# Kernel optimization log

Hardware: AMD Instinct MI355X
Metric: run time of the kernel (lower is better)

The kernel has to match this reference:

```python
import jax, jax.numpy as jnp
import numpy as np

N, E, D, H, O, L = 50000, 400000, 128, 128, 64, 2


def setup_inputs() -> dict:
    key = jax.random.key(0)
    ks = jax.random.split(key, 24)
    s = 0.05
    rn = lambda k, shape: jax.random.normal(k, shape, jnp.float32) * s
    # random edges with no self-loops (dst = src + nonzero offset mod N)
    src = jax.random.randint(ks[0], (E,), 0, N, dtype=jnp.int32)
    off = jax.random.randint(ks[1], (E,), 1, N, dtype=jnp.int32)
    dst = (src + off) % N
    edge_index = jnp.stack([src, dst])  # [2, E] int32
    return {
        "x": rn(ks[2], (N, D)),
        "edge_index": edge_index,
        "attn_W": rn(ks[3], (L, 2 * D, 2)),
        "attn_b": rn(ks[4], (L, 2)),
        "mlp_W1": rn(ks[5], (L, D, H)),
        "mlp_b1": rn(ks[6], (L, H)),
        "mlp_W2": rn(ks[7], (L, H, H)),
        "mlp_b2": rn(ks[8], (L, H)),
        "bn_gamma": jnp.ones((L, H), jnp.float32),   # torch BatchNorm1d default affine init
        "bn_beta": jnp.zeros((L, H), jnp.float32),
        "gru_Wih": rn(ks[9], (D, 3 * H)),
        "gru_Whh": rn(ks[10], (H, 3 * H)),
        "gru_bih": rn(ks[11], (3 * H,)),
        "gru_bhh": rn(ks[12], (3 * H,)),
        "last_W1": rn(ks[13], (H, H)),
        "last_b1": rn(ks[14], (H,)),
        "last_W2": rn(ks[15], (H, O)),
        "last_b2": rn(ks[16], (O,)),
    }


def reference(x, edge_index, attn_W, attn_b, mlp_W1, mlp_b1, mlp_W2, mlp_b2,
              bn_gamma, bn_beta, gru_Wih, gru_Whh, gru_bih, gru_bhh,
              last_W1, last_b1, last_W2, last_b2):
    n = x.shape[0]
    # symmetrize edge list: message (nbr -> node) for both directions
    node = jnp.concatenate([edge_index[0], edge_index[1]])  # destination
    nbr = jnp.concatenate([edge_index[1], edge_index[0]])   # source / neighbor
    deg = jax.ops.segment_sum(jnp.ones((node.shape[0], 1), x.dtype), node, num_segments=n)
    has_nbr = deg > 0

    h_state = jnp.zeros((n, gru_Whh.shape[0]), x.dtype)
    for l in range(attn_W.shape[0]):
        feats = x[nbr]  # [2E, d] gather
        s_agg = jax.ops.segment_sum(feats, node, num_segments=n)
        m_agg = jax.ops.segment_max(feats, node, num_segments=n)
        m_agg = jnp.where(has_nbr, m_agg, jnp.zeros_like(m_agg))  # isolated nodes stay 0
        # attention over {sum, max} aggregations
        scores = jnp.concatenate([s_agg, m_agg], axis=1) @ attn_W[l] + attn_b[l]  # [n, 2]
        w = jax.nn.softmax(scores, axis=1)
        comb = x + w[:, :1] * s_agg + w[:, 1:] * m_agg
        # MLP (in -> hidden, ReLU, hidden -> out)
        z = jax.nn.relu(comb @ mlp_W1[l] + mlp_b1[l]) @ mlp_W2[l] + mlp_b2[l]
        # BatchNorm1d in eval mode with running stats (mean 0, var 1): affine only
        z = z * bn_gamma[l] + bn_beta[l]
        # GRUCell
        gi = z @ gru_Wih + gru_bih
        gh = h_state @ gru_Whh + gru_bhh
        ir, iz, inn = jnp.split(gi, 3, axis=1)
        hr, hz, hn = jnp.split(gh, 3, axis=1)
        r = jax.nn.sigmoid(ir + hr)
        u = jax.nn.sigmoid(iz + hz)
        ncand = jnp.tanh(inn + r * hn)
        h_state = (1.0 - u) * ncand + u * h_state
        x = h_state
    # final node-level MLP
    out = jax.nn.relu(x @ last_W1 + last_b1) @ last_W2 + last_b2
    return out
```

## Files before the change

kernel.cpp:

```cpp
#include <hip/hip_runtime.h>
#include <math.h>

typedef unsigned short u16;
typedef __attribute__((ext_vector_type(8))) short bf16x8;
typedef __attribute__((ext_vector_type(4))) float f32x4;

#define ADJ_CAP 96

__device__ __forceinline__ u16 f2b(float f) {
    union { float f; unsigned u; } v; v.f = f;
    unsigned r = (v.u + 0x7FFF + ((v.u >> 16) & 1)) >> 16;
    return (u16)r;
}
__device__ __forceinline__ float b2f(u16 h) {
    union { unsigned u; float f; } v; v.u = (unsigned)h << 16;
    return v.f;
}
__device__ __forceinline__ float u2f(unsigned u) {
    union { unsigned u; float f; } v; v.u = u;
    return v.f;
}
__device__ __forceinline__ float fsig(float x) { return 1.f / (1.f + __expf(-x)); }
__device__ __forceinline__ float ftanh(float x) {
    float e = __expf(2.f * x);
    return 1.f - 2.f / (e + 1.f);
}

__device__ __forceinline__ void gll16(const void* g, void* l) {
    __builtin_amdgcn_global_load_lds(
        (const __attribute__((address_space(1))) void*)g,
        (__attribute__((address_space(3))) void*)l, 16, 0, 0);
}

__device__ __forceinline__ void conv_chunk(const float* __restrict__ src,
                                           u16* __restrict__ dst, int c, int NC) {
    int sl = c / NC, n = c - sl * NC;
    u16 tmp[8];
#pragma unroll
    for (int i = 0; i < 8; ++i) tmp[i] = f2b(src[(size_t)(sl * 8 + i) * NC + n]);
    *(uint4*)(dst + (size_t)c * 8) = *(const uint4*)tmp;
}

__global__ void k_pro(const int* __restrict__ ei, int* __restrict__ cnt,
                      u16* __restrict__ adj, int E, int N,
                      const float* __restrict__ W1, const float* __restrict__ W2,
                      const float* __restrict__ Wih, const float* __restrict__ Whh,
                      const float* __restrict__ lW1, const float* __restrict__ lW2,
                      u16* __restrict__ tW1, u16* __restrict__ tW2,
                      u16* __restrict__ tGRU,
                      u16* __restrict__ tlW1, u16* __restrict__ tlW2, int L,
                      const float* __restrict__ x, u16* __restrict__ xb, int n8) {
    const int EB = (E + 255) >> 8;
    const int nwc = L * 4096 + 12288 + 3072;
    const int WB = (nwc + 255) >> 8;
    int b = blockIdx.x;
    if (b < EB * 8) {
        const int part = b & 7, chunk = b >> 3;
        const int span = (N + 7) >> 3;
        const int nlo = part * span;
        const int nhi = (nlo + span < N) ? nlo + span : N;
        int e = chunk * 256 + threadIdx.x;
        if (e < E) {
            int s = __builtin_nontemporal_load(&ei[e]);
            int d = __builtin_nontemporal_load(&ei[E + e]);
            if (s >= nlo && s < nhi) {
                int p = atomicAdd(&cnt[s], 1);
                adj[(size_t)s * ADJ_CAP + p] = (u16)d;
            }
            if (d >= nlo && d < nhi) {
                int q = atomicAdd(&cnt[d], 1);
                adj[(size_t)d * ADJ_CAP + q] = (u16)s;
            }
        }
        return;
    }
    b -= EB * 8;
    if (b < WB) {
        int c = b * 256 + threadIdx.x;
        if (c >= nwc) return;
        if (c < L * 2048) { int l = c >> 11; conv_chunk(W1 + (size_t)l * 16384, tW1 + (size_t)l * 16384, c & 2047, 128); return; }
        c -= L * 2048;
        if (c < L * 2048) { int l = c >> 11; conv_chunk(W2 + (size_t)l * 16384, tW2 + (size_t)l * 16384, c & 2047, 128); return; }
        c -= L * 2048;
        if (c < 12288) {
            int s = c >> 9, r = c & 511;
            int q = r >> 7, mat = (r >> 6) & 1, cc = r & 63;
            int h = s / 12, s2 = s % 12, kc = s2 / 3, g = s2 % 3;
            int ocol = g * 128 + h * 64 + cc;
            const float* src = mat ? Whh : Wih;
            int kb = (kc * 4 + q) * 8;
            u16 tmp[8];
#pragma unroll
            for (int e = 0; e < 8; ++e) tmp[e] = f2b(src[(size_t)(kb + e) * 384 + ocol]);
            *(uint4*)(tGRU + (size_t)c * 8) = *(const uint4*)tmp;
            return;
        }
        c -= 12288;
        if (c < 2048) { conv_chunk(lW1, tlW1, c, 128); return; }
        c -= 2048;
        if (c < 1024) { conv_chunk(lW2, tlW2, c, 64); return; }
        return;
    }
    b -= WB;
    {
        int i = b * 256 + threadIdx.x;
        if (i < n8) {
            float4 a = *(const float4*)(x + (size_t)i * 8);
            float4 bb = *(const float4*)(x + (size_t)i * 8 + 4);
            u16 t[8] = {f2b(a.x), f2b(a.y), f2b(a.z), f2b(a.w),
                        f2b(bb.x), f2b(bb.y), f2b(bb.z), f2b(bb.w)};
            *(uint4*)(xb + (size_t)i * 8) = *(const uint4*)t;
        }
    }
}

__global__ __launch_bounds__(256) void k_agg(const u16* __restrict__ xb,
                                             const u16* __restrict__ adj,
                                             const int* __restrict__ cnt,
                                             const float* __restrict__ aW,
                                             const float* __restrict__ ab,
                                             u16* __restrict__ comb, int N) {
    int n = blockIdx.x * 4 + (threadIdx.x >> 6);
    if (n >= N) return;
    int l = threadIdx.x & 63;
    int grp = l >> 4;
    int f0 = (l & 15) * 8;
    int beg = n * ADJ_CAP, deg = cnt[n], end = beg + deg;
    float s[8], m[8];
#pragma unroll
    for (int i = 0; i < 8; ++i) { s[i] = 0.f; m[i] = -3.402823e38f; }

    auto acc8 = [&](uint4 v) {
        unsigned d[4] = {v.x, v.y, v.z, v.w};
#pragma unroll
        for (int i = 0; i < 4; ++i) {
            float a0 = u2f(d[i] << 16);
            float a1 = u2f(d[i] & 0xFFFF0000u);
            s[2 * i] += a0;     m[2 * i] = fmaxf(m[2 * i], a0);
            s[2 * i + 1] += a1; m[2 * i + 1] = fmaxf(m[2 * i + 1], a1);
        }
    };

    int j = beg + grp;
    for (; j + 4 < end; j += 8) {
        int a0 = adj[j], a1 = adj[j + 4];
        uint4 v0 = *(const uint4*)(xb + (size_t)a0 * 128 + f0);
        uint4 v1 = *(const uint4*)(xb + (size_t)a1 * 128 + f0);
        acc8(v0);
        acc8(v1);
    }
    if (j < end) {
        int a = adj[j];
        uint4 v = *(const uint4*)(xb + (size_t)a * 128 + f0);
        acc8(v);
    }
#pragma unroll
    for (int i = 0; i < 8; ++i) {
        s[i] += __shfl_xor(s[i], 16);
        s[i] += __shfl_xor(s[i], 32);
        m[i] = fmaxf(m[i], __shfl_xor(m[i], 16));
        m[i] = fmaxf(m[i], __shfl_xor(m[i], 32));
    }
    if (deg == 0) {
#pragma unroll
        for (int i = 0; i < 8; ++i) m[i] = 0.f;
    }
    float p0 = 0.f, p1 = 0.f;
#pragma unroll
    for (int i = 0; i < 8; ++i) {
        float2 wS = *(const float2*)(aW + (size_t)(f0 + i) * 2);
        float2 wM = *(const float2*)(aW + (size_t)(128 + f0 + i) * 2);
        p0 += s[i] * wS.x + m[i] * wM.x;
        p1 += s[i] * wS.y + m[i] * wM.y;
    }
#pragma unroll
    for (int o = 8; o; o >>= 1) { p0 += __shfl_xor(p0, o); p1 += __shfl_xor(p1, o); }
    p0 += ab[0]; p1 += ab[1];
    float pm = fmaxf(p0, p1);
    float ea = __expf(p0 - pm), eb = __expf(p1 - pm);
    float w0 = ea / (ea + eb), w1 = 1.f - w0;
    if (grp == 0) {
        uint4 xv = *(const uint4*)(xb + (size_t)n * 128 + f0);
        unsigned xs[4] = {xv.x, xv.y, xv.z, xv.w};
        unsigned dw[4];
#pragma unroll
        for (int i = 0; i < 4; ++i) {
            float xlo = u2f(xs[i] << 16), xhi = u2f(xs[i] & 0xFFFF0000u);
            float olo = xlo + w0 * s[2 * i] + w1 * m[2 * i];
            float ohi = xhi + w0 * s[2 * i + 1] + w1 * m[2 * i + 1];
            dw[i] = (unsigned)f2b(olo) | ((unsigned)f2b(ohi) << 16);
        }
        uint4 o4 = make_uint4(dw[0], dw[1], dw[2], dw[3]);
        *(uint4*)(comb + (size_t)n * 128 + f0) = o4;
    }
}

template <bool H0>
__global__ __launch_bounds__(512, 4) void k_layer(
    const u16* __restrict__ Cb, const u16* __restrict__ Hb,
    const u16* __restrict__ W1t, const float* __restrict__ b1,
    const u16* __restrict__ W2t, const float* __restrict__ b2,
    const float* __restrict__ gam, const float* __restrict__ bet,
    const u16* __restrict__ tG,
    const float* __restrict__ bih, const float* __restrict__ bhh,
    u16* __restrict__ HnB, int M) {
    __shared__ __align__(16) u16 x_s[128 * 16 * 8];
    __shared__ __align__(16) u16 b_s[3][4096];
    const int t = threadIdx.x;
    const int m0 = blockIdx.x * 128;
    const int wid = t >> 6, lane = t & 63, lo = lane & 15, hi = lane >> 4;
    const int arow = 16 * wid + lo;

    auto issue = [&](int s) {
        const u16* g = (s < 4) ? (W1t + (size_t)s * 4096)
                     : (s < 8) ? (W2t + (size_t)(s - 4) * 4096)
                               : (tG + (size_t)(s - 8) * 4096);
        char* l = (char*)b_s[s % 3] + wid * 1024;
        const char* gp = (const char*)g + wid * 1024 + lane * 16;
        gll16(gp, l);
    };

    float b1r[8], g2r[8], t2r[8];
#pragma unroll
    for (int j = 0; j < 8; ++j) {
        int c = 16 * j + lo;
        b1r[j] = b1[c];
        float gv = gam[c];
        g2r[j] = gv;
        t2r[j] = b2[c] * gv + bet[c];
    }
#pragma unroll
    for (int i = 0; i < 4; ++i) {
        int off = (i * 8 + wid) * 1024;
        int row = (off >> 8) + (lane >> 4);
        int sl = lane & 15;
        int gr = m0 + row; gr = gr < M ? gr : M - 1;
        gll16(Cb + (size_t)gr * 128 + ((sl ^ (row & 7)) * 8), (char*)x_s + off);
    }
    issue(0);
    issue(1);

    f32x4 acc[8];
#pragma unroll
    for (int j = 0; j < 8; ++j) acc[j] = (f32x4)0.f;

#pragma unroll
    for (int ks = 0; ks < 4; ++ks) {
        const int p = ks;
        asm volatile("s_waitcnt vmcnt(1)" ::: "memory");
        __builtin_amdgcn_s_barrier();
        issue(p + 2);
        bf16x8 af = *(const bf16x8*)&x_s[(arow * 16 + ((ks * 4 + hi) ^ (arow & 7))) * 8];
        const u16* buf = b_s[p % 3];
        __builtin_amdgcn_s_setprio(1);
#pragma unroll
        for (int j = 0; j < 8; ++j) {
            bf16x8 bf = *(const bf16x8*)&buf[((size_t)hi * 128 + 16 * j + lo) * 8];
            acc[j] = __builtin_amdgcn_mfma_f32_16x16x32_bf16(af, bf, acc[j], 0, 0, 0);
        }
        __builtin_amdgcn_s_setprio(0);
    }
#pragma unroll
    for (int j = 0; j < 8; ++j) {
        int c = 16 * j + lo;
#pragma unroll
        for (int q = 0; q < 4; ++q) {
            int row = 16 * wid + hi * 4 + q;
            float v = fmaxf(acc[j][q] + b1r[j], 0.f);
            int sl = c >> 3;
            x_s[(row * 16 + (sl ^ (row & 7))) * 8 + (c & 7)] = f2b(v);
        }
        acc[j] = (f32x4)0.f;
    }

#pragma unroll
    for (int ks = 0; ks < 4; ++ks) {
        const int p = 4 + ks;
        asm volatile("s_waitcnt vmcnt(1)" ::: "memory");
        __builtin_amdgcn_s_barrier();
        issue(p + 2);
        bf16x8 af = *(const bf16x8*)&x_s[(arow * 16 + ((ks * 4 + hi) ^ (arow & 7))) * 8];
        const u16* buf = b_s[p % 3];
        __builtin_amdgcn_s_setprio(1);
#pragma unroll
        for (int j = 0; j < 8; ++j) {
            bf16x8 bf = *(const bf16x8*)&buf[((size_t)hi * 128 + 16 * j + lo) * 8];
            acc[j] = __builtin_amdgcn_mfma_f32_16x16x32_bf16(af, bf, acc[j], 0, 0, 0);
        }
        __builtin_amdgcn_s_setprio(0);
    }
#pragma unroll
    for (int j = 0; j < 8; ++j) {
        int c = 16 * j + lo;
#pragma unroll
        for (int q = 0; q < 4; ++q) {
            int row = 16 * wid + hi * 4 + q;
            float v = acc[j][q] * g2r[j] + t2r[j];
            int sl = c >> 3;
            x_s[(row * 16 + (sl ^ (row & 7))) * 8 + (c & 7)] = f2b(v);
        }
    }
    bf16x8 hreg[4];
    if (!H0) {
        int gr = m0 + arow; gr = gr < M ? gr : M - 1;
#pragma unroll
        for (int kc = 0; kc < 4; ++kc)
            hreg[kc] = *(const bf16x8*)(Hb + (size_t)gr * 128 + (kc * 4 + hi) * 8);
    }

    f32x4 racc[4], uacc[4], nza[4], nha[4];

    auto epi = [&](int h) {
#pragma unroll
        for (int ct = 0; ct < 4; ++ct) {
            int c = h * 64 + ct * 16 + lo;
            float b_r = bih[c] + bhh[c];
            float b_u = bih[c + 128] + bhh[c + 128];
            float b_in = bih[c + 256], b_hn = bhh[c + 256];
#pragma unroll
            for (int q = 0; q < 4; ++q) {
                int r = m0 + 16 * wid + hi * 4 + q;
                if (r < M) {
                    float rr = fsig(racc[ct][q] + b_r);
                    float uu = fsig(uacc[ct][q] + b_u);
                    float hterm = H0 ? b_hn : (nha[ct][q] + b_hn);
                    float nn = ftanh(nza[ct][q] + b_in + rr * hterm);
                    float hv = H0 ? 0.f : b2f(Hb[(size_t)r * 128 + c]);
                    float o = (1.f - uu) * nn + uu * hv;
                    HnB[(size_t)r * 128 + c] = f2b(o);
                }
            }
        }
    };

#pragma unroll
    for (int h = 0; h < 2; ++h) {
#pragma unroll
        for (int j = 0; j < 4; ++j) {
            racc[j] = (f32x4)0.f; uacc[j] = (f32x4)0.f;
            nza[j] = (f32x4)0.f; nha[j] = (f32x4)0.f;
        }
#pragma unroll
        for (int kc = 0; kc < 4; ++kc) {
            bf16x8 zf;
#pragma unroll
            for (int g = 0; g < 3; ++g) {
                const int p = 8 + h * 12 + kc * 3 + g;
                if (p == 31) asm volatile("s_waitcnt vmcnt(0)" ::: "memory");
                else         asm volatile("s_waitcnt vmcnt(1)" ::: "memory");
                __builtin_amdgcn_s_barrier();
                if (p + 2 <= 31) issue(p + 2);
                if (g == 0)
                    zf = *(const bf16x8*)&x_s[(arow * 16 + ((kc * 4 + hi) ^ (arow & 7))) * 8];
                const u16* buf = b_s[p % 3];
                __builtin_amdgcn_s_setprio(1);
#pragma unroll
                for (int jj = 0; jj < 4; ++jj) {
                    bf16x8 wi = *(const bf16x8*)&buf[((size_t)hi * 128 + jj * 16 + lo) * 8];
                    if (g == 0)      racc[jj] = __builtin_amdgcn_mfma_f32_16x16x32_bf16(zf, wi, racc[jj], 0, 0, 0);
                    else if (g == 1) uacc[jj] = __builtin_amdgcn_mfma_f32_16x16x32_bf16(zf, wi, uacc[jj], 0, 0, 0);
                    else             nza[jj]  = __builtin_amdgcn_mfma_f32_16x16x32_bf16(zf, wi, nza[jj], 0, 0, 0);
                    if (!H0) {
                        bf16x8 wh = *(const bf16x8*)&buf[((size_t)hi * 128 + 64 + jj * 16 + lo) * 8];
                        if (g == 0)      racc[jj] = __builtin_amdgcn_mfma_f32_16x16x32_bf16(hreg[kc], wh, racc[jj], 0, 0, 0);
                        else if (g == 1) uacc[jj] = __builtin_amdgcn_mfma_f32_16x16x32_bf16(hreg[kc], wh, uacc[jj], 0, 0, 0);
                        else             nha[jj]  = __builtin_amdgcn_mfma_f32_16x16x32_bf16(hreg[kc], wh, nha[jj], 0, 0, 0);
                    }
                }
                __builtin_amdgcn_s_setprio(0);
            }
        }
        epi(h);
    }
}

__global__ __launch_bounds__(256, 2) void k_final(const u16* __restrict__ Hb,
                                                  const u16* __restrict__ W1t,
                                                  const float* __restrict__ b1,
                                                  const u16* __restrict__ W2t,
                                                  const float* __restrict__ b2,
                                                  float* __restrict__ out, int M) {
    __shared__ __align__(16) u16 x_s[64 * 16 * 8];
    __shared__ __align__(16) u16 w_s[16 * 128 * 8];
    const int t = threadIdx.x;
    const int m0 = blockIdx.x * 64;
    const int w = t >> 6, l = t & 63, lo = l & 15, hi = l >> 4;
    const int arow = 16 * w + lo;
#pragma unroll
    for (int i = 0; i < 4; ++i) {
        int idx = t + i * 256;
        int row = idx >> 4, sl = idx & 15;
        int gr = m0 + row; gr = gr < M ? gr : M - 1;
        *(uint4*)&x_s[(row * 16 + (sl ^ (row & 7))) * 8] =
            *(const uint4*)(Hb + (size_t)gr * 128 + sl * 8);
    }
#pragma unroll
    for (int i = 0; i < 8; ++i) {
        int idx = t + i * 256;
        *(uint4*)&w_s[idx * 8] = *(const uint4*)(W1t + (size_t)idx * 8);
    }
    __syncthreads();
    f32x4 acc[8];
#pragma unroll
    for (int j = 0; j < 8; ++j) acc[j] = (f32x4)0.f;
#pragma unroll
    for (int ks = 0; ks < 4; ++ks) {
        bf16x8 af = *(const bf16x8*)&x_s[(arow * 16 + ((ks * 4 + hi) ^ (arow & 7))) * 8];
#pragma unroll
        for (int j = 0; j < 8; ++j) {
            bf16x8 bf = *(const bf16x8*)&w_s[((ks * 4 + hi) * 128 + 16 * j + lo) * 8];
            acc[j] = __builtin_amdgcn_mfma_f32_16x16x32_bf16(af, bf, acc[j], 0, 0, 0);
        }
    }
    __syncthreads();
#pragma unroll
    for (int j = 0; j < 8; ++j) {
        int c = 16 * j + lo;
        float bv = b1[c];
#pragma unroll
        for (int q = 0; q < 4; ++q) {
            int row = 16 * w + hi * 4 + q;
            float v = fmaxf(acc[j][q] + bv, 0.f);
            int sl = c >> 3;
            x_s[(row * 16 + (sl ^ (row & 7))) * 8 + (c & 7)] = f2b(v);
        }
    }
#pragma unroll
    for (int i = 0; i < 4; ++i) {
        int idx = t + i * 256;
        *(uint4*)&w_s[idx * 8] = *(const uint4*)(W2t + (size_t)idx * 8);
    }
    __syncthreads();
    f32x4 a2[4];
#pragma unroll
    for (int j = 0; j < 4; ++j) a2[j] = (f32x4)0.f;
#pragma unroll
    for (int ks = 0; ks < 4; ++ks) {
        bf16x8 af = *(const bf16x8*)&x_s[(arow * 16 + ((ks * 4 + hi) ^ (arow & 7))) * 8];
#pragma unroll
        for (int j = 0; j < 4; ++j) {
            bf16x8 bf = *(const bf16x8*)&w_s[((ks * 4 + hi) * 64 + 16 * j + lo) * 8];
            a2[j] = __builtin_amdgcn_mfma_f32_16x16x32_bf16(af, bf, a2[j], 0, 0, 0);
        }
    }
#pragma unroll
    for (int j = 0; j < 4; ++j) {
        int c = 16 * j + lo;
        float bv = b2[c];
#pragma unroll
        for (int q = 0; q < 4; ++q) {
            int r = m0 + 16 * w + hi * 4 + q;
            if (r < M) out[(size_t)r * 64 + c] = a2[j][q] + bv;
        }
    }
}

extern "C" void kernel_launch(void* const* d_in, const int* in_sizes, int n_in,
                              void* d_out, int out_size, void* d_ws, size_t ws_size,
                              hipStream_t stream) {
    const float* x   = (const float*)d_in[0];
    const int*   ei  = (const int*)d_in[1];
    const float* aW  = (const float*)d_in[2];
    const float* ab  = (const float*)d_in[3];
    const float* W1  = (const float*)d_in[4];
    const float* b1  = (const float*)d_in[5];
    const float* W2  = (const float*)d_in[6];
    const float* b2  = (const float*)d_in[7];
    const float* gam = (const float*)d_in[8];
    const float* bet = (const float*)d_in[9];
    const float* Wih = (const float*)d_in[10];
    const float* Whh = (const float*)d_in[11];
    const float* bih = (const float*)d_in[12];
    const float* bhh = (const float*)d_in[13];
    const float* lW1 = (const float*)d_in[14];
    const float* lb1 = (const float*)d_in[15];
    const float* lW2 = (const float*)d_in[16];
    const float* lb2 = (const float*)d_in[17];

    const int N = in_sizes[0] / 128;
    const int E = in_sizes[1] / 2;
    const int L = in_sizes[3] / 2;
    float* out = (float*)d_out;

    char* ws = (char*)d_ws;
    size_t off = 0;
    auto alloc = [&](size_t bytes) -> void* {
        void* p = ws + off;
        off = (off + bytes + 255) & ~(size_t)255;
        return p;
    };
    int* cnt  = (int*)alloc((size_t)N * 4);
    u16* adj  = (u16*)alloc((size_t)N * ADJ_CAP * 2);
    u16* tW1  = (u16*)alloc((size_t)L * 16384 * 2);
    u16* tW2  = (u16*)alloc((size_t)L * 16384 * 2);
    u16* tGRU = (u16*)alloc((size_t)98304 * 2);
    u16* tlW1 = (u16*)alloc((size_t)16384 * 2);
    u16* tlW2 = (u16*)alloc((size_t)8192 * 2);
    u16* xb   = (u16*)alloc((size_t)N * 128 * 2);
    u16* comb = (u16*)alloc((size_t)N * 128 * 2);
    u16* hAb  = (u16*)alloc((size_t)N * 128 * 2);
    u16* hBb  = (u16*)alloc((size_t)N * 128 * 2);
    (void)ws_size; (void)n_in; (void)out_size;

    hipMemsetAsync(cnt, 0, (size_t)N * 4, stream);

    const int EB = (E + 255) / 256;
    const int nwc = L * 4096 + 12288 + 3072;
    const int WB = (nwc + 255) / 256;
    const int FB = (N * 16 + 255) / 256;
    k_pro<<<EB * 8 + WB + FB, 256, 0, stream>>>(ei, cnt, adj, E, N,
                                                W1, W2, Wih, Whh, lW1, lW2,
                                                tW1, tW2, tGRU, tlW1, tlW2, L,
                                                x, xb, N * 16);

    const int mb = (N + 127) / 128;
    k_agg<<<(N + 3) / 4, 256, 0, stream>>>(xb, adj, cnt, aW, ab, comb, N);
    k_layer<true><<<mb, 512, 0, stream>>>(
        comb, nullptr, tW1, b1, tW2, b2, gam, bet,
        tGRU, bih, bhh, hAb, N);
    k_agg<<<(N + 3) / 4, 256, 0, stream>>>(hAb, adj, cnt, aW + 512, ab + 2, comb, N);
    k_layer<false><<<mb, 512, 0, stream>>>(
        comb, hAb, tW1 + 16384, b1 + 128, tW2 + 16384, b2 + 128,
        gam + 128, bet + 128, tGRU, bih, bhh, hBb, N);

    k_final<<<(N + 63) / 64, 256, 0, stream>>>(hBb, tlW1, lb1, tlW2, lb2, out, N);
}
```

Measured before the change: 222.0 us.

## Fuse neighbor aggregation into the per-layer MLP/GRU kernel via LDS tile

Removes the separate aggregation kernel and the comb buffer. Each layer block now gathers neighbors for its own 64-row tile and writes the attention-combined rows straight into shared memory before the MLP and GRU MFMA stages. To fit this, blocks shrink to 256 threads and 64 rows, and each wave loads twice as much of the weight staging per issue, with the vmcnt waits adjusted to match. This saves a global write and read of the combined features and one launch per layer. The cost is a serialized per-wave gather loop ahead of the matmuls and smaller tiles that reload the weights more often.

```diff
diff --git a/kernel.cpp b/kernel.cpp
--- a/kernel.cpp
+++ b/kernel.cpp
@@ -114,100 +114,21 @@
     }
 }
 
-__global__ __launch_bounds__(256) void k_agg(const u16* __restrict__ xb,
-                                             const u16* __restrict__ adj,
-                                             const int* __restrict__ cnt,
-                                             const float* __restrict__ aW,
-                                             const float* __restrict__ ab,
-                                             u16* __restrict__ comb, int N) {
-    int n = blockIdx.x * 4 + (threadIdx.x >> 6);
-    if (n >= N) return;
-    int l = threadIdx.x & 63;
-    int grp = l >> 4;
-    int f0 = (l & 15) * 8;
-    int beg = n * ADJ_CAP, deg = cnt[n], end = beg + deg;
-    float s[8], m[8];
-#pragma unroll
-    for (int i = 0; i < 8; ++i) { s[i] = 0.f; m[i] = -3.402823e38f; }
-
-    auto acc8 = [&](uint4 v) {
-        unsigned d[4] = {v.x, v.y, v.z, v.w};
-#pragma unroll
-        for (int i = 0; i < 4; ++i) {
-            float a0 = u2f(d[i] << 16);
-            float a1 = u2f(d[i] & 0xFFFF0000u);
-            s[2 * i] += a0;     m[2 * i] = fmaxf(m[2 * i], a0);
-            s[2 * i + 1] += a1; m[2 * i + 1] = fmaxf(m[2 * i + 1], a1);
-        }
-    };
-
-    int j = beg + grp;
-    for (; j + 4 < end; j += 8) {
-        int a0 = adj[j], a1 = adj[j + 4];
-        uint4 v0 = *(const uint4*)(xb + (size_t)a0 * 128 + f0);
-        uint4 v1 = *(const uint4*)(xb + (size_t)a1 * 128 + f0);
-        acc8(v0);
-        acc8(v1);
-    }
-    if (j < end) {
-        int a = adj[j];
-        uint4 v = *(const uint4*)(xb + (size_t)a * 128 + f0);
-        acc8(v);
-    }
-#pragma unroll
-    for (int i = 0; i < 8; ++i) {
-        s[i] += __shfl_xor(s[i], 16);
-        s[i] += __shfl_xor(s[i], 32);
-        m[i] = fmaxf(m[i], __shfl_xor(m[i], 16));
-        m[i] = fmaxf(m[i], __shfl_xor(m[i], 32));
-    }
-    if (deg == 0) {
-#pragma unroll
-        for (int i = 0; i < 8; ++i) m[i] = 0.f;
-    }
-    float p0 = 0.f, p1 = 0.f;
-#pragma unroll
-    for (int i = 0; i < 8; ++i) {
-        float2 wS = *(const float2*)(aW + (size_t)(f0 + i) * 2);
-        float2 wM = *(const float2*)(aW + (size_t)(128 + f0 + i) * 2);
-        p0 += s[i] * wS.x + m[i] * wM.x;
-        p1 += s[i] * wS.y + m[i] * wM.y;
-    }
-#pragma unroll
-    for (int o = 8; o; o >>= 1) { p0 += __shfl_xor(p0, o); p1 += __shfl_xor(p1, o); }
-    p0 += ab[0]; p1 += ab[1];
-    float pm = fmaxf(p0, p1);
-    float ea = __expf(p0 - pm), eb = __expf(p1 - pm);
-    float w0 = ea / (ea + eb), w1 = 1.f - w0;
-    if (grp == 0) {
-        uint4 xv = *(const uint4*)(xb + (size_t)n * 128 + f0);
-        unsigned xs[4] = {xv.x, xv.y, xv.z, xv.w};
-        unsigned dw[4];
-#pragma unroll
-        for (int i = 0; i < 4; ++i) {
-            float xlo = u2f(xs[i] << 16), xhi = u2f(xs[i] & 0xFFFF0000u);
-            float olo = xlo + w0 * s[2 * i] + w1 * m[2 * i];
-            float ohi = xhi + w0 * s[2 * i + 1] + w1 * m[2 * i + 1];
-            dw[i] = (unsigned)f2b(olo) | ((unsigned)f2b(ohi) << 16);
-        }
-        uint4 o4 = make_uint4(dw[0], dw[1], dw[2], dw[3]);
-        *(uint4*)(comb + (size_t)n * 128 + f0) = o4;
-    }
-}
-
 template <bool H0>
-__global__ __launch_bounds__(512, 4) void k_layer(
-    const u16* __restrict__ Cb, const u16* __restrict__ Hb,
+__global__ __launch_bounds__(256, 4) void k_flayer(
+    const u16* __restrict__ xin, const u16* __restrict__ adj,
+    const int* __restrict__ cnt,
+    const float* __restrict__ aW, const float* __restrict__ ab,
     const u16* __restrict__ W1t, const float* __restrict__ b1,
     const u16* __restrict__ W2t, const float* __restrict__ b2,
     const float* __restrict__ gam, const float* __restrict__ bet,
     const u16* __restrict__ tG,
     const float* __restrict__ bih, const float* __restrict__ bhh,
     u16* __restrict__ HnB, int M) {
-    __shared__ __align__(16) u16 x_s[128 * 16 * 8];
+    __shared__ __align__(16) u16 x_s[64 * 16 * 8];
     __shared__ __align__(16) u16 b_s[3][4096];
     const int t = threadIdx.x;
-    const int m0 = blockIdx.x * 128;
+    const int m0 = blockIdx.x * 64;
     const int wid = t >> 6, lane = t & 63, lo = lane & 15, hi = lane >> 4;
     const int arow = 16 * wid + lo;
 
@@ -215,10 +136,91 @@
         const u16* g = (s < 4) ? (W1t + (size_t)s * 4096)
                      : (s < 8) ? (W2t + (size_t)(s - 4) * 4096)
                                : (tG + (size_t)(s - 8) * 4096);
-        char* l = (char*)b_s[s % 3] + wid * 1024;
-        const char* gp = (const char*)g + wid * 1024 + lane * 16;
+        char* l = (char*)b_s[s % 3] + wid * 2048;
+        const char* gp = (const char*)g + wid * 2048 + lane * 16;
         gll16(gp, l);
+        gll16(gp + 1024, l + 1024);
     };
+
+    issue(0);
+    issue(1);
+
+    {
+        const int grp = lane >> 4;
+        const int f0 = lo * 8;
+#pragma unroll 1
+        for (int i = 0; i < 16; ++i) {
+            int n = m0 + 16 * wid + i;
+            n = n < M ? n : M - 1;
+            int deg = cnt[n];
+            int beg = n * ADJ_CAP, end = beg + deg;
+            float s[8], m[8];
+#pragma unroll
+            for (int k = 0; k < 8; ++k) { s[k] = 0.f; m[k] = -3.402823e38f; }
+            auto acc8 = [&](uint4 v) {
+                unsigned d[4] = {v.x, v.y, v.z, v.w};
+#pragma unroll
+                for (int k = 0; k < 4; ++k) {
+                    float a0 = u2f(d[k] << 16);
+                    float a1 = u2f(d[k] & 0xFFFF0000u);
+                    s[2 * k] += a0;     m[2 * k] = fmaxf(m[2 * k], a0);
+                    s[2 * k + 1] += a1; m[2 * k + 1] = fmaxf(m[2 * k + 1], a1);
+                }
+            };
+            int j = beg + grp;
+            for (; j + 4 < end; j += 8) {
+                int a0 = adj[j], a1 = adj[j + 4];
+                uint4 v0 = *(const uint4*)(xin + (size_t)a0 * 128 + f0);
+                uint4 v1 = *(const uint4*)(xin + (size_t)a1 * 128 + f0);
+                acc8(v0);
+                acc8(v1);
+            }
+            if (j < end) {
+                int a = adj[j];
+                acc8(*(const uint4*)(xin + (size_t)a * 128 + f0));
+            }
+#pragma unroll
+            for (int k = 0; k < 8; ++k) {
+                s[k] += __shfl_xor(s[k], 16);
+                s[k] += __shfl_xor(s[k], 32);
+                m[k] = fmaxf(m[k], __shfl_xor(m[k], 16));
+                m[k] = fmaxf(m[k], __shfl_xor(m[k], 32));
+            }
+            if (deg == 0) {
+#pragma unroll
+                for (int k = 0; k < 8; ++k) m[k] = 0.f;
+            }
+            float p0 = 0.f, p1 = 0.f;
+#pragma unroll
+            for (int k = 0; k < 8; ++k) {
+                float2 wS = *(const float2*)(aW + (size_t)(f0 + k) * 2);
+                float2 wM = *(const float2*)(aW + (size_t)(128 + f0 + k) * 2);
+                p0 += s[k] * wS.x + m[k] * wM.x;
+                p1 += s[k] * wS.y + m[k] * wM.y;
+            }
+#pragma unroll
+            for (int o = 8; o; o >>= 1) { p0 += __shfl_xor(p0, o); p1 += __shfl_xor(p1, o); }
+            p0 += ab[0]; p1 += ab[1];
+            float pm = fmaxf(p0, p1);
+            float ea = __expf(p0 - pm), eb = __expf(p1 - pm);
+            float w0 = ea / (ea + eb), w1 = 1.f - w0;
+            if (grp == 0) {
+                uint4 xv = *(const uint4*)(xin + (size_t)n * 128 + f0);
+                unsigned xs4[4] = {xv.x, xv.y, xv.z, xv.w};
+                unsigned dw[4];
+#pragma unroll
+                for (int k = 0; k < 4; ++k) {
+                    float xlo = u2f(xs4[k] << 16), xhi = u2f(xs4[k] & 0xFFFF0000u);
+                    float olo = xlo + w0 * s[2 * k] + w1 * m[2 * k];
+                    float ohi = xhi + w0 * s[2 * k + 1] + w1 * m[2 * k + 1];
+                    dw[k] = (unsigned)f2b(olo) | ((unsigned)f2b(ohi) << 16);
+                }
+                int row = 16 * wid + i;
+                uint4 o4 = make_uint4(dw[0], dw[1], dw[2], dw[3]);
+                *(uint4*)&x_s[(row * 16 + (lo ^ (row & 7))) * 8] = o4;
+            }
+        }
+    }
 
     float b1r[8], g2r[8], t2r[8];
 #pragma unroll
@@ -229,16 +231,6 @@
         g2r[j] = gv;
         t2r[j] = b2[c] * gv + bet[c];
     }
-#pragma unroll
-    for (int i = 0; i < 4; ++i) {
-        int off = (i * 8 + wid) * 1024;
-        int row = (off >> 8) + (lane >> 4);
-        int sl = lane & 15;
-        int gr = m0 + row; gr = gr < M ? gr : M - 1;
-        gll16(Cb + (size_t)gr * 128 + ((sl ^ (row & 7)) * 8), (char*)x_s + off);
-    }
-    issue(0);
-    issue(1);
 
     f32x4 acc[8];
 #pragma unroll
@@ -247,7 +239,7 @@
 #pragma unroll
     for (int ks = 0; ks < 4; ++ks) {
         const int p = ks;
-        asm volatile("s_waitcnt vmcnt(1)" ::: "memory");
+        asm volatile("s_waitcnt vmcnt(2)" ::: "memory");
         __builtin_amdgcn_s_barrier();
         issue(p + 2);
         bf16x8 af = *(const bf16x8*)&x_s[(arow * 16 + ((ks * 4 + hi) ^ (arow & 7))) * 8];
@@ -276,7 +268,7 @@
 #pragma unroll
     for (int ks = 0; ks < 4; ++ks) {
         const int p = 4 + ks;
-        asm volatile("s_waitcnt vmcnt(1)" ::: "memory");
+        asm volatile("s_waitcnt vmcnt(2)" ::: "memory");
         __builtin_amdgcn_s_barrier();
         issue(p + 2);
         bf16x8 af = *(const bf16x8*)&x_s[(arow * 16 + ((ks * 4 + hi) ^ (arow & 7))) * 8];
@@ -305,7 +297,7 @@
         int gr = m0 + arow; gr = gr < M ? gr : M - 1;
 #pragma unroll
         for (int kc = 0; kc < 4; ++kc)
-            hreg[kc] = *(const bf16x8*)(Hb + (size_t)gr * 128 + (kc * 4 + hi) * 8);
+            hreg[kc] = *(const bf16x8*)(xin + (size_t)gr * 128 + (kc * 4 + hi) * 8);
     }
 
     f32x4 racc[4], uacc[4], nza[4], nha[4];
@@ -325,7 +317,7 @@
                     float uu = fsig(uacc[ct][q] + b_u);
                     float hterm = H0 ? b_hn : (nha[ct][q] + b_hn);
                     float nn = ftanh(nza[ct][q] + b_in + rr * hterm);
-                    float hv = H0 ? 0.f : b2f(Hb[(size_t)r * 128 + c]);
+                    float hv = H0 ? 0.f : b2f(xin[(size_t)r * 128 + c]);
                     float o = (1.f - uu) * nn + uu * hv;
                     HnB[(size_t)r * 128 + c] = f2b(o);
                 }
@@ -347,7 +339,7 @@
             for (int g = 0; g < 3; ++g) {
                 const int p = 8 + h * 12 + kc * 3 + g;
                 if (p == 31) asm volatile("s_waitcnt vmcnt(0)" ::: "memory");
-                else         asm volatile("s_waitcnt vmcnt(1)" ::: "memory");
+                else         asm volatile("s_waitcnt vmcnt(2)" ::: "memory");
                 __builtin_amdgcn_s_barrier();
                 if (p + 2 <= 31) issue(p + 2);
                 if (g == 0)
@@ -497,7 +489,6 @@
     u16* tlW1 = (u16*)alloc((size_t)16384 * 2);
     u16* tlW2 = (u16*)alloc((size_t)8192 * 2);
     u16* xb   = (u16*)alloc((size_t)N * 128 * 2);
-    u16* comb = (u16*)alloc((size_t)N * 128 * 2);
     u16* hAb  = (u16*)alloc((size_t)N * 128 * 2);
     u16* hBb  = (u16*)alloc((size_t)N * 128 * 2);
     (void)ws_size; (void)n_in; (void)out_size;
@@ -513,14 +504,14 @@
                                                 tW1, tW2, tGRU, tlW1, tlW2, L,
                                                 x, xb, N * 16);
 
-    const int mb = (N + 127) / 128;
-    k_agg<<<(N + 3) / 4, 256, 0, stream>>>(xb, adj, cnt, aW, ab, comb, N);
-    k_layer<true><<<mb, 512, 0, stream>>>(
-        comb, nullptr, tW1, b1, tW2, b2, gam, bet,
+    const int mb = (N + 63) / 64;
+    k_flayer<true><<<mb, 256, 0, stream>>>(
+        xb, adj, cnt, aW, ab,
+        tW1, b1, tW2, b2, gam, bet,
         tGRU, bih, bhh, hAb, N);
-    k_agg<<<(N + 3) / 4, 256, 0, stream>>>(hAb, adj, cnt, aW + 512, ab + 2, comb, N);
-    k_layer<false><<<mb, 512, 0, stream>>>(
-        comb, hAb, tW1 + 16384, b1 + 128, tW2 + 16384, b2 + 128,
+    k_flayer<false><<<mb, 256, 0, stream>>>(
+        hAb, adj, cnt, aW + 512, ab + 2,
+        tW1 + 16384, b1 + 128, tW2 + 16384, b2 + 128,
         gam + 128, bet + 128, tGRU, bih, bhh, hBb, N);
 
     k_final<<<(N + 63) / 64, 256, 0, stream>>>(hBb, tlW1, lb1, tlW2, lb2, out, N);
```

After: 242.5 us. 9.2% more time.
